# Optimization experiments

Measured on AMD Instinct MI355X. Metric: run time of the kernel, lower is better.

The kernel has to match this reference:

```python
import jax, jax.numpy as jnp
import numpy as np

N = 50000   # num nodes
D = 64      # feature dim
R = 4       # num relations (len(adjs))
E = 800000  # edges per relation (avg degree 16)


def setup_inputs() -> dict:
    key = jax.random.key(0)
    k0, k1, k2, k3, k4 = jax.random.split(key, 5)
    x = jax.random.normal(k0, (N, D), dtype=jnp.float32)
    weight = jax.random.normal(k1, (R,), dtype=jnp.float32)        # scalar weight per relation
    edge_vals = jax.random.uniform(k2, (R, E), dtype=jnp.float32)  # nonzero values of adjs
    edge_rows = jax.random.randint(k3, (R, E), 0, N)               # COO row (destination) indices
    edge_cols = jax.random.randint(k4, (R, E), 0, N)               # COO col (source) indices
    return {"x": x, "weight": weight, "edge_vals": edge_vals,
            "edge_rows": edge_rows, "edge_cols": edge_cols, "idx": 1}


def reference(x, weight, edge_vals, edge_rows, edge_cols, idx):
    # spmm(adjs[idx], x): gather source features, scale by edge values, scatter-add to rows
    rows = edge_rows[idx]
    cols = edge_cols[idx]
    vals = edge_vals[idx]
    msgs = vals[:, None] * x[cols]                                  # [E, D]
    agg = jax.ops.segment_sum(msgs, rows, num_segments=N)           # [N, D]
    return weight[idx] * agg
```

## Files before the change

kernel.cpp:

```cpp
#include <hip/hip_runtime.h>


#define FEAT_D 64
#define BROWS 64
#define BSH 6
#define MAXBKT 1024
#define LCAP 44
#define OVFCAP 16384
#define EPB 4096
#define BBLOCK 512
#define EPT (EPB / BBLOCK)
#define GBLOCK 512

__global__ __launch_bounds__(BBLOCK) void build_kernel(
        const float* __restrict__ edge_vals,
        const int* __restrict__ edge_rows,
        const int* __restrict__ edge_cols,
        const int* __restrict__ idx_ptr,
        int* __restrict__ bktcnt,
        int2* __restrict__ pack,
        int* __restrict__ ovfcnt,
        int4* __restrict__ ovfbuf,
        int E, int NBKT, int cap) {
    __shared__ int2 stage[EPB];
    __shared__ unsigned short sbkt[EPB];
    __shared__ int lh[MAXBKT];
    __shared__ int lofs[MAXBKT];
    __shared__ int gbase[MAXBKT];
    __shared__ int ssum[BBLOCK];
    const long long off = (long long)idx_ptr[0] * E;
    const int* rows = edge_rows + off;
    const int* cols = edge_cols + off;
    const float* vals = edge_vals + off;
    const int t = threadIdx.x;
    const int s = blockIdx.x * EPB;
    const int e2 = min(s + EPB, E);
    const int cnt_total = e2 - s;

    for (int k = t; k < NBKT; k += BBLOCK) lh[k] = 0;
    __syncthreads();

    int2 myrec[EPT];
    int mybkt[EPT];
#pragma unroll
    for (int k = 0; k < EPT; ++k) {
        const int g = s + t + k * BBLOCK;
        mybkt[k] = -1;
        if (g < e2) {
            const int r = rows[g];
            const int c = cols[g];
            const float v = vals[g];
            mybkt[k] = r >> BSH;
            myrec[k] = make_int2((c << BSH) | (r & (BROWS - 1)), __float_as_int(v));
            atomicAdd(&lh[mybkt[k]], 1);
        }
    }
    __syncthreads();

    const int i0 = 2 * t, i1 = 2 * t + 1;
    const int a0 = (i0 < NBKT) ? lh[i0] : 0;
    const int a1 = (i1 < NBKT) ? lh[i1] : 0;
    ssum[t] = a0 + a1;
    __syncthreads();
    for (int d = 1; d < BBLOCK; d <<= 1) {
        const int add = (t >= d) ? ssum[t - d] : 0;
        __syncthreads();
        ssum[t] += add;
        __syncthreads();
    }
    const int exc = ssum[t] - (a0 + a1);
    if (i0 < NBKT) lofs[i0] = exc;
    if (i1 < NBKT) lofs[i1] = exc + a0;
    __syncthreads();

    for (int k = t; k < NBKT; k += BBLOCK) lh[k] = lofs[k];
    __syncthreads();

#pragma unroll
    for (int k = 0; k < EPT; ++k) {
        if (mybkt[k] >= 0) {
            const int pos = atomicAdd(&lh[mybkt[k]], 1);
            stage[pos] = myrec[k];
            sbkt[pos] = (unsigned short)mybkt[k];
        }
    }
    __syncthreads();

    for (int k = t; k < NBKT; k += BBLOCK) {
        const int c = lh[k] - lofs[k];
        gbase[k] = (c > 0) ? atomicAdd(&bktcnt[k], c) : 0;
    }
    __syncthreads();

    for (int p = t; p < cnt_total; p += BBLOCK) {
        const int k = sbkt[p];
        const int g = gbase[k] + (p - lofs[k]);
        const int2 rec = stage[p];
        if (g < cap) {
            __builtin_nontemporal_store(
                *(const long long*)&rec,
                (long long*)(pack + (long long)k * cap + g));
        } else {
            const int o = atomicAdd(ovfcnt, 1);
            if (o < OVFCAP)
                ovfbuf[o] = make_int4((k << BSH) | (rec.x & (BROWS - 1)),
                                      rec.x >> BSH, rec.y, 0);
        }
    }
}

__global__ __launch_bounds__(GBLOCK) void gather_kernel(
        const float* __restrict__ x,
        const float* __restrict__ weight,
        const int* __restrict__ idx_ptr,
        const int* __restrict__ bktcnt,
        const int2* __restrict__ pack,
        int* __restrict__ ovfcnt, int4* __restrict__ ovfbuf,
        float* __restrict__ out, int N, int cap) {
    __shared__ int2 slist[BROWS * LCAP];
    __shared__ int scur[BROWS];
    const int b = blockIdx.x;
    const int t = threadIdx.x;
    const int w = t >> 6;
    const int lane = t & 63;
    if (t < BROWS) scur[t] = 0;
    __syncthreads();
    const int cnt = min(bktcnt[b], cap);
    const long long* psrc = (const long long*)(pack + (long long)b * cap);
    for (int j = t; j < cnt; j += GBLOCK) {
        const long long raw = __builtin_nontemporal_load(psrc + j);
        const int2 rec = make_int2((int)(unsigned)raw, (int)(raw >> 32));
        const int rl = rec.x & (BROWS - 1);
        const int li = atomicAdd(&scur[rl], 1);
        if (li < LCAP) {
            slist[rl * LCAP + li] = rec;
        } else {
            const int o = atomicAdd(ovfcnt, 1);
            if (o < OVFCAP)
                ovfbuf[o] = make_int4((b << BSH) | rl, rec.x >> BSH, rec.y, 0);
        }
    }
    __syncthreads();
    const float ws = weight[idx_ptr[0]];
    float acc[8];
#pragma unroll
    for (int q = 0; q < 8; ++q) acc[q] = 0.f;
#pragma unroll
    for (int q = 0; q < 8; ++q) {
        const int rl = w * 8 + q;
        const int n = min(scur[rl], LCAP);
        const int2* lp = slist + rl * LCAP;
        int j = 0;
        for (; j + 4 <= n; j += 4) {
            const int2 r0 = lp[j], r1 = lp[j + 1], r2 = lp[j + 2], r3 = lp[j + 3];
            const float x0 = x[(r0.x >> BSH) * FEAT_D + lane];
            const float x1 = x[(r1.x >> BSH) * FEAT_D + lane];
            const float x2 = x[(r2.x >> BSH) * FEAT_D + lane];
            const float x3 = x[(r3.x >> BSH) * FEAT_D + lane];
            acc[q] += __int_as_float(r0.y) * x0 + __int_as_float(r1.y) * x1 +
                      __int_as_float(r2.y) * x2 + __int_as_float(r3.y) * x3;
        }
        for (; j < n; ++j) {
            const int2 r0 = lp[j];
            acc[q] += __int_as_float(r0.y) * x[(r0.x >> BSH) * FEAT_D + lane];
        }
    }
    const int row0 = (b << BSH) + w * 8;
#pragma unroll
    for (int q = 0; q < 8; ++q) {
        const int row = row0 + q;
        if (row < N)
            __builtin_nontemporal_store(ws * acc[q],
                                        &out[(long long)row * FEAT_D + lane]);
    }
}

__global__ void fixup_kernel(const float* __restrict__ x,
                             const float* __restrict__ weight,
                             const int* __restrict__ idx_ptr,
                             const int* __restrict__ ovfcnt,
                             const int4* __restrict__ ovfbuf,
                             float* __restrict__ out) {
    const int n = min(*ovfcnt, OVFCAP);
    if (n == 0) return;
    const float ws = weight[idx_ptr[0]];
    const int gw = (int)((blockIdx.x * (long long)blockDim.x + threadIdx.x) >> 6);
    const int lane = threadIdx.x & 63;
    const int nw = (gridDim.x * blockDim.x) >> 6;
    for (int r = gw; r < n; r += nw) {
        const int4 rec = ovfbuf[r];
        atomicAdd(&out[(long long)rec.x * FEAT_D + lane],
                  ws * __int_as_float(rec.z) * x[(long long)rec.y * FEAT_D + lane]);
    }
}

__global__ void spmm_scatter_kernel(const float* __restrict__ x,
                                    const float* __restrict__ weight,
                                    const float* __restrict__ edge_vals,
                                    const int* __restrict__ edge_rows,
                                    const int* __restrict__ edge_cols,
                                    const int* __restrict__ idx_ptr,
                                    float* __restrict__ out,
                                    int E, long long work) {
    const int idx = idx_ptr[0];
    const float w = weight[idx];
    const long long rel_off = (long long)idx * E;
    long long t = (long long)blockIdx.x * blockDim.x + threadIdx.x;
    if (t >= work) return;
    const int e = (int)(t >> 4);
    const int q = (int)(t & 15);
    const int r = edge_rows[rel_off + e];
    const int c = edge_cols[rel_off + e];
    const float wv = w * edge_vals[rel_off + e];
    const float4 xv = *reinterpret_cast<const float4*>(x + (long long)c * FEAT_D + q * 4);
    float* op = out + (long long)r * FEAT_D + q * 4;
    atomicAdd(op + 0, wv * xv.x);
    atomicAdd(op + 1, wv * xv.y);
    atomicAdd(op + 2, wv * xv.z);
    atomicAdd(op + 3, wv * xv.w);
}

extern "C" void kernel_launch(void* const* d_in, const int* in_sizes, int n_in,
                              void* d_out, int out_size, void* d_ws, size_t ws_size,
                              hipStream_t stream) {
    const float* x         = (const float*)d_in[0];
    const float* weight    = (const float*)d_in[1];
    const float* edge_vals = (const float*)d_in[2];
    const int*   edge_rows = (const int*)d_in[3];
    const int*   edge_cols = (const int*)d_in[4];
    const int*   idx_ptr   = (const int*)d_in[5];
    float* out = (float*)d_out;

    const int R = in_sizes[1];
    const int E = in_sizes[2] / R;
    const int N = in_sizes[0] / FEAT_D;
    const int NBKT = (N + BROWS - 1) >> BSH;

    char* ws = (char*)d_ws;
    size_t o_bktcnt = 0;
    size_t o_ovfcnt = o_bktcnt + (size_t)NBKT * 4;
    size_t o_ovfbuf = ((o_ovfcnt + 4 + 15) / 16) * 16;
    size_t o_pack   = o_ovfbuf + (size_t)OVFCAP * 16;
    const size_t room = (ws_size > o_pack) ? (ws_size - o_pack) : 0;
    int cap = (int)(room / ((size_t)NBKT * 8));
    if (cap > 2048) cap = 2048;

    const long long meanload = (NBKT > 0) ? ((long long)E / NBKT) : 0;
    if (cap < 128 || cap < meanload + (meanload >> 3) + 32 || NBKT > MAXBKT) {
        hipMemsetAsync(d_out, 0, (size_t)out_size * sizeof(float), stream);
        const long long work = (long long)E * 16;
        const int block = 256;
        const long long grid = (work + block - 1) / block;
        spmm_scatter_kernel<<<dim3((unsigned)grid), dim3(block), 0, stream>>>(
            x, weight, edge_vals, edge_rows, edge_cols, idx_ptr, out, E, work);
        return;
    }

    int*  bktcnt = (int*)(ws + o_bktcnt);
    int*  ovfcnt = (int*)(ws + o_ovfcnt);
    int4* ovfbuf = (int4*)(ws + o_ovfbuf);
    int2* pack   = (int2*)(ws + o_pack);

    hipMemsetAsync(bktcnt, 0, (size_t)NBKT * 4 + 4, stream);

    const int bgrid = (E + EPB - 1) / EPB;
    build_kernel<<<bgrid, BBLOCK, 0, stream>>>(edge_vals, edge_rows,
                                               edge_cols, idx_ptr, bktcnt,
                                               pack, ovfcnt, ovfbuf,
                                               E, NBKT, cap);

    gather_kernel<<<NBKT, GBLOCK, 0, stream>>>(x, weight, idx_ptr, bktcnt,
                                               pack, ovfcnt, ovfbuf,
                                               out, N, cap);

    fixup_kernel<<<64, 256, 0, stream>>>(x, weight, idx_ptr, ovfcnt, ovfbuf, out);
}
```

Baseline: 135.6 us.

## Split gather buckets across two blocks, deepen unroll, halve build tile

The gather kernel now launches two 256-thread blocks per 64-row bucket. Each block scans the whole bucket list but keeps only the records for its 32-row half, which halves shared memory per block and raises occupancy through launch bounds. The inner accumulation loop gets an 8-way unrolled stage so more independent x loads are in flight. The build kernel uses 2048 edges per block, giving more blocks. The trade-off is that each bucket's pack list is read twice and the build kernel does more global atomics.

```diff
diff --git a/kernel.cpp b/kernel.cpp
--- a/kernel.cpp
+++ b/kernel.cpp
@@ -7,10 +7,10 @@
 #define MAXBKT 1024
 #define LCAP 44
 #define OVFCAP 16384
-#define EPB 4096
+#define EPB 2048
 #define BBLOCK 512
 #define EPT (EPB / BBLOCK)
-#define GBLOCK 512
+#define GBLOCK 256
 
 __global__ __launch_bounds__(BBLOCK) void build_kernel(
         const float* __restrict__ edge_vals,
@@ -109,7 +109,7 @@
     }
 }
 
-__global__ __launch_bounds__(GBLOCK) void gather_kernel(
+__global__ __launch_bounds__(GBLOCK, 8) void gather_kernel(
         const float* __restrict__ x,
         const float* __restrict__ weight,
         const int* __restrict__ idx_ptr,
@@ -117,13 +117,14 @@
         const int2* __restrict__ pack,
         int* __restrict__ ovfcnt, int4* __restrict__ ovfbuf,
         float* __restrict__ out, int N, int cap) {
-    __shared__ int2 slist[BROWS * LCAP];
-    __shared__ int scur[BROWS];
-    const int b = blockIdx.x;
+    __shared__ int2 slist[32 * LCAP];
+    __shared__ int scur[32];
+    const int b = blockIdx.x >> 1;
+    const int half = blockIdx.x & 1;
     const int t = threadIdx.x;
     const int w = t >> 6;
     const int lane = t & 63;
-    if (t < BROWS) scur[t] = 0;
+    if (t < 32) scur[t] = 0;
     __syncthreads();
     const int cnt = min(bktcnt[b], cap);
     const long long* psrc = (const long long*)(pack + (long long)b * cap);
@@ -131,13 +132,16 @@
         const long long raw = __builtin_nontemporal_load(psrc + j);
         const int2 rec = make_int2((int)(unsigned)raw, (int)(raw >> 32));
         const int rl = rec.x & (BROWS - 1);
-        const int li = atomicAdd(&scur[rl], 1);
-        if (li < LCAP) {
-            slist[rl * LCAP + li] = rec;
-        } else {
-            const int o = atomicAdd(ovfcnt, 1);
-            if (o < OVFCAP)
-                ovfbuf[o] = make_int4((b << BSH) | rl, rec.x >> BSH, rec.y, 0);
+        if ((rl >> 5) == half) {
+            const int lrl = rl & 31;
+            const int li = atomicAdd(&scur[lrl], 1);
+            if (li < LCAP) {
+                slist[lrl * LCAP + li] = rec;
+            } else {
+                const int o = atomicAdd(ovfcnt, 1);
+                if (o < OVFCAP)
+                    ovfbuf[o] = make_int4((b << BSH) | rl, rec.x >> BSH, rec.y, 0);
+            }
         }
     }
     __syncthreads();
@@ -147,10 +151,27 @@
     for (int q = 0; q < 8; ++q) acc[q] = 0.f;
 #pragma unroll
     for (int q = 0; q < 8; ++q) {
-        const int rl = w * 8 + q;
-        const int n = min(scur[rl], LCAP);
-        const int2* lp = slist + rl * LCAP;
+        const int lrl = w * 8 + q;
+        const int n = min(scur[lrl], LCAP);
+        const int2* lp = slist + lrl * LCAP;
         int j = 0;
+        for (; j + 8 <= n; j += 8) {
+            const int2 r0 = lp[j],     r1 = lp[j + 1], r2 = lp[j + 2],
+                       r3 = lp[j + 3], r4 = lp[j + 4], r5 = lp[j + 5],
+                       r6 = lp[j + 6], r7 = lp[j + 7];
+            const float x0 = x[(r0.x >> BSH) * FEAT_D + lane];
+            const float x1 = x[(r1.x >> BSH) * FEAT_D + lane];
+            const float x2 = x[(r2.x >> BSH) * FEAT_D + lane];
+            const float x3 = x[(r3.x >> BSH) * FEAT_D + lane];
+            const float x4 = x[(r4.x >> BSH) * FEAT_D + lane];
+            const float x5 = x[(r5.x >> BSH) * FEAT_D + lane];
+            const float x6 = x[(r6.x >> BSH) * FEAT_D + lane];
+            const float x7 = x[(r7.x >> BSH) * FEAT_D + lane];
+            acc[q] += __int_as_float(r0.y) * x0 + __int_as_float(r1.y) * x1 +
+                      __int_as_float(r2.y) * x2 + __int_as_float(r3.y) * x3 +
+                      __int_as_float(r4.y) * x4 + __int_as_float(r5.y) * x5 +
+                      __int_as_float(r6.y) * x6 + __int_as_float(r7.y) * x7;
+        }
         for (; j + 4 <= n; j += 4) {
             const int2 r0 = lp[j], r1 = lp[j + 1], r2 = lp[j + 2], r3 = lp[j + 3];
             const float x0 = x[(r0.x >> BSH) * FEAT_D + lane];
@@ -165,7 +186,7 @@
             acc[q] += __int_as_float(r0.y) * x[(r0.x >> BSH) * FEAT_D + lane];
         }
     }
-    const int row0 = (b << BSH) + w * 8;
+    const int row0 = (b << BSH) + half * 32 + w * 8;
 #pragma unroll
     for (int q = 0; q < 8; ++q) {
         const int row = row0 + q;
@@ -269,9 +290,9 @@
                                                pack, ovfcnt, ovfbuf,
                                                E, NBKT, cap);
 
-    gather_kernel<<<NBKT, GBLOCK, 0, stream>>>(x, weight, idx_ptr, bktcnt,
-                                               pack, ovfcnt, ovfbuf,
-                                               out, N, cap);
+    gather_kernel<<<NBKT * 2, GBLOCK, 0, stream>>>(x, weight, idx_ptr, bktcnt,
+                                                   pack, ovfcnt, ovfbuf,
+                                                   out, N, cap);
 
     fixup_kernel<<<64, 256, 0, stream>>>(x, weight, idx_ptr, ovfcnt, ovfbuf, out);
 }
```

Result: slower. 140.1 us (+3.3%).

## Write per-chunk sorted edge runs with offset tables instead of global bucket atomics

Applied to the files above, without the earlier changes.

The build kernel now writes each chunk's locally bucket-sorted edges contiguously, along with a per-chunk table of 16-bit bucket offsets. This replaces the global atomic bucket counters, the scattered writes into fixed-capacity bucket slots, the memset and the capacity overflow path. The gather kernel walks all chunks' offset tables to collect its bucket's edges, trading coalesced build writes for many small scattered reads in gather. The inner gather loop is also unrolled to 8 edges, and ovfcnt is now reset inside the build kernel.

```diff
diff --git a/kernel.cpp b/kernel.cpp
--- a/kernel.cpp
+++ b/kernel.cpp
@@ -17,27 +17,26 @@
         const int* __restrict__ edge_rows,
         const int* __restrict__ edge_cols,
         const int* __restrict__ idx_ptr,
-        int* __restrict__ bktcnt,
         int2* __restrict__ pack,
+        unsigned short* __restrict__ ofs,
         int* __restrict__ ovfcnt,
-        int4* __restrict__ ovfbuf,
-        int E, int NBKT, int cap) {
+        int E, int NBKT) {
     __shared__ int2 stage[EPB];
-    __shared__ unsigned short sbkt[EPB];
     __shared__ int lh[MAXBKT];
     __shared__ int lofs[MAXBKT];
-    __shared__ int gbase[MAXBKT];
     __shared__ int ssum[BBLOCK];
     const long long off = (long long)idx_ptr[0] * E;
     const int* rows = edge_rows + off;
     const int* cols = edge_cols + off;
     const float* vals = edge_vals + off;
     const int t = threadIdx.x;
-    const int s = blockIdx.x * EPB;
+    const int c = blockIdx.x;
+    const int s = c * EPB;
     const int e2 = min(s + EPB, E);
     const int cnt_total = e2 - s;
 
     for (int k = t; k < NBKT; k += BBLOCK) lh[k] = 0;
+    if (c == 0 && t == 0) *ovfcnt = 0;
     __syncthreads();
 
     int2 myrec[EPT];
@@ -48,10 +47,10 @@
         mybkt[k] = -1;
         if (g < e2) {
             const int r = rows[g];
-            const int c = cols[g];
+            const int col = cols[g];
             const float v = vals[g];
             mybkt[k] = r >> BSH;
-            myrec[k] = make_int2((c << BSH) | (r & (BROWS - 1)), __float_as_int(v));
+            myrec[k] = make_int2((col << BSH) | (r & (BROWS - 1)), __float_as_int(v));
             atomicAdd(&lh[mybkt[k]], 1);
         }
     }
@@ -81,42 +80,28 @@
         if (mybkt[k] >= 0) {
             const int pos = atomicAdd(&lh[mybkt[k]], 1);
             stage[pos] = myrec[k];
-            sbkt[pos] = (unsigned short)mybkt[k];
-        }
-    }
-    __syncthreads();
-
-    for (int k = t; k < NBKT; k += BBLOCK) {
-        const int c = lh[k] - lofs[k];
-        gbase[k] = (c > 0) ? atomicAdd(&bktcnt[k], c) : 0;
-    }
-    __syncthreads();
-
-    for (int p = t; p < cnt_total; p += BBLOCK) {
-        const int k = sbkt[p];
-        const int g = gbase[k] + (p - lofs[k]);
-        const int2 rec = stage[p];
-        if (g < cap) {
-            __builtin_nontemporal_store(
-                *(const long long*)&rec,
-                (long long*)(pack + (long long)k * cap + g));
-        } else {
-            const int o = atomicAdd(ovfcnt, 1);
-            if (o < OVFCAP)
-                ovfbuf[o] = make_int4((k << BSH) | (rec.x & (BROWS - 1)),
-                                      rec.x >> BSH, rec.y, 0);
-        }
-    }
+        }
+    }
+    __syncthreads();
+
+    unsigned short* orow = ofs + (long long)c * (NBKT + 1);
+    for (int k = t; k < NBKT; k += BBLOCK) orow[k] = (unsigned short)lofs[k];
+    if (t == 0) orow[NBKT] = (unsigned short)cnt_total;
+
+    long long* dst = (long long*)(pack + (long long)c * EPB);
+    const long long* src = (const long long*)stage;
+    for (int p = t; p < cnt_total; p += BBLOCK)
+        __builtin_nontemporal_store(src[p], dst + p);
 }
 
 __global__ __launch_bounds__(GBLOCK) void gather_kernel(
         const float* __restrict__ x,
         const float* __restrict__ weight,
         const int* __restrict__ idx_ptr,
-        const int* __restrict__ bktcnt,
         const int2* __restrict__ pack,
+        const unsigned short* __restrict__ ofs,
         int* __restrict__ ovfcnt, int4* __restrict__ ovfbuf,
-        float* __restrict__ out, int N, int cap) {
+        float* __restrict__ out, int N, int NBKT, int nchunks) {
     __shared__ int2 slist[BROWS * LCAP];
     __shared__ int scur[BROWS];
     const int b = blockIdx.x;
@@ -125,19 +110,23 @@
     const int lane = t & 63;
     if (t < BROWS) scur[t] = 0;
     __syncthreads();
-    const int cnt = min(bktcnt[b], cap);
-    const long long* psrc = (const long long*)(pack + (long long)b * cap);
-    for (int j = t; j < cnt; j += GBLOCK) {
-        const long long raw = __builtin_nontemporal_load(psrc + j);
-        const int2 rec = make_int2((int)(unsigned)raw, (int)(raw >> 32));
-        const int rl = rec.x & (BROWS - 1);
-        const int li = atomicAdd(&scur[rl], 1);
-        if (li < LCAP) {
-            slist[rl * LCAP + li] = rec;
-        } else {
-            const int o = atomicAdd(ovfcnt, 1);
-            if (o < OVFCAP)
-                ovfbuf[o] = make_int4((b << BSH) | rl, rec.x >> BSH, rec.y, 0);
+    for (int c = t; c < nchunks; c += GBLOCK) {
+        const unsigned short* op = ofs + (long long)c * (NBKT + 1) + b;
+        const int rs = op[0];
+        const int re = op[1];
+        const long long* psrc = (const long long*)(pack + (long long)c * EPB);
+        for (int p = rs; p < re; ++p) {
+            const long long raw = __builtin_nontemporal_load(psrc + p);
+            const int2 rec = make_int2((int)(unsigned)raw, (int)(raw >> 32));
+            const int rl = rec.x & (BROWS - 1);
+            const int li = atomicAdd(&scur[rl], 1);
+            if (li < LCAP) {
+                slist[rl * LCAP + li] = rec;
+            } else {
+                const int o = atomicAdd(ovfcnt, 1);
+                if (o < OVFCAP)
+                    ovfbuf[o] = make_int4((b << BSH) | rl, rec.x >> BSH, rec.y, 0);
+            }
         }
     }
     __syncthreads();
@@ -151,6 +140,23 @@
         const int n = min(scur[rl], LCAP);
         const int2* lp = slist + rl * LCAP;
         int j = 0;
+        for (; j + 8 <= n; j += 8) {
+            const int2 r0 = lp[j],     r1 = lp[j + 1], r2 = lp[j + 2],
+                       r3 = lp[j + 3], r4 = lp[j + 4], r5 = lp[j + 5],
+                       r6 = lp[j + 6], r7 = lp[j + 7];
+            const float x0 = x[(r0.x >> BSH) * FEAT_D + lane];
+            const float x1 = x[(r1.x >> BSH) * FEAT_D + lane];
+            const float x2 = x[(r2.x >> BSH) * FEAT_D + lane];
+            const float x3 = x[(r3.x >> BSH) * FEAT_D + lane];
+            const float x4 = x[(r4.x >> BSH) * FEAT_D + lane];
+            const float x5 = x[(r5.x >> BSH) * FEAT_D + lane];
+            const float x6 = x[(r6.x >> BSH) * FEAT_D + lane];
+            const float x7 = x[(r7.x >> BSH) * FEAT_D + lane];
+            acc[q] += __int_as_float(r0.y) * x0 + __int_as_float(r1.y) * x1 +
+                      __int_as_float(r2.y) * x2 + __int_as_float(r3.y) * x3 +
+                      __int_as_float(r4.y) * x4 + __int_as_float(r5.y) * x5 +
+                      __int_as_float(r6.y) * x6 + __int_as_float(r7.y) * x7;
+        }
         for (; j + 4 <= n; j += 4) {
             const int2 r0 = lp[j], r1 = lp[j + 1], r2 = lp[j + 2], r3 = lp[j + 3];
             const float x0 = x[(r0.x >> BSH) * FEAT_D + lane];
@@ -235,18 +241,16 @@
     const int E = in_sizes[2] / R;
     const int N = in_sizes[0] / FEAT_D;
     const int NBKT = (N + BROWS - 1) >> BSH;
+    const int nchunks = (E + EPB - 1) / EPB;
 
     char* ws = (char*)d_ws;
-    size_t o_bktcnt = 0;
-    size_t o_ovfcnt = o_bktcnt + (size_t)NBKT * 4;
+    size_t o_pack   = 0;
+    size_t o_ofs    = o_pack + (size_t)nchunks * EPB * 8;
+    size_t o_ovfcnt = o_ofs + (((size_t)nchunks * (NBKT + 1) * 2 + 7) & ~(size_t)7);
     size_t o_ovfbuf = ((o_ovfcnt + 4 + 15) / 16) * 16;
-    size_t o_pack   = o_ovfbuf + (size_t)OVFCAP * 16;
-    const size_t room = (ws_size > o_pack) ? (ws_size - o_pack) : 0;
-    int cap = (int)(room / ((size_t)NBKT * 8));
-    if (cap > 2048) cap = 2048;
-
-    const long long meanload = (NBKT > 0) ? ((long long)E / NBKT) : 0;
-    if (cap < 128 || cap < meanload + (meanload >> 3) + 32 || NBKT > MAXBKT) {
+    size_t needed   = o_ovfbuf + (size_t)OVFCAP * 16;
+
+    if (ws_size < needed || NBKT > MAXBKT || N > MAXBKT * BROWS) {
         hipMemsetAsync(d_out, 0, (size_t)out_size * sizeof(float), stream);
         const long long work = (long long)E * 16;
         const int block = 256;
@@ -256,22 +260,18 @@
         return;
     }
 
-    int*  bktcnt = (int*)(ws + o_bktcnt);
-    int*  ovfcnt = (int*)(ws + o_ovfcnt);
-    int4* ovfbuf = (int4*)(ws + o_ovfbuf);
-    int2* pack   = (int2*)(ws + o_pack);
-
-    hipMemsetAsync(bktcnt, 0, (size_t)NBKT * 4 + 4, stream);
-
-    const int bgrid = (E + EPB - 1) / EPB;
-    build_kernel<<<bgrid, BBLOCK, 0, stream>>>(edge_vals, edge_rows,
-                                               edge_cols, idx_ptr, bktcnt,
-                                               pack, ovfcnt, ovfbuf,
-                                               E, NBKT, cap);
-
-    gather_kernel<<<NBKT, GBLOCK, 0, stream>>>(x, weight, idx_ptr, bktcnt,
-                                               pack, ovfcnt, ovfbuf,
-                                               out, N, cap);
+    int2*           pack   = (int2*)(ws + o_pack);
+    unsigned short* ofs    = (unsigned short*)(ws + o_ofs);
+    int*            ovfcnt = (int*)(ws + o_ovfcnt);
+    int4*           ovfbuf = (int4*)(ws + o_ovfbuf);
+
+    build_kernel<<<nchunks, BBLOCK, 0, stream>>>(edge_vals, edge_rows,
+                                                 edge_cols, idx_ptr,
+                                                 pack, ofs, ovfcnt, E, NBKT);
+
+    gather_kernel<<<NBKT, GBLOCK, 0, stream>>>(x, weight, idx_ptr, pack, ofs,
+                                               ovfcnt, ovfbuf, out, N, NBKT,
+                                               nchunks);
 
     fixup_kernel<<<64, 256, 0, stream>>>(x, weight, idx_ptr, ovfcnt, ovfbuf, out);
 }
```

Result: no change. 136.0 us (+0.3%).
